# Optimization experiments

Hardware: AMD Instinct MI355X
Metric: run time of the kernel (lower is better)

## Reference

```python
import jax, jax.numpy as jnp
import numpy as np

N_NODES = 50000
N_EDGES = 1_600_000
D_IN, D_HID, D_OUT, K = 128, 50, 10, 5


def setup_inputs() -> dict:
    key = jax.random.key(0)
    ks = jax.random.split(key, 6)
    x = jax.random.normal(ks[0], (N_NODES, D_IN), dtype=jnp.float32)
    edge_index = jax.random.randint(ks[1], (2, N_EDGES), 0, N_NODES, dtype=jnp.int64)
    cheb_w = jax.random.normal(ks[2], (K, D_IN, D_HID), dtype=jnp.float32) * 0.05
    cheb_b = jax.random.normal(ks[3], (D_HID,), dtype=jnp.float32) * 0.05
    fc_w = jax.random.normal(ks[4], (D_HID, D_OUT), dtype=jnp.float32) * 0.1
    fc_b = jax.random.normal(ks[5], (D_OUT,), dtype=jnp.float32) * 0.1
    return {"x": x, "edge_index": edge_index, "cheb_w": cheb_w,
            "cheb_b": cheb_b, "fc_w": fc_w, "fc_b": fc_b}


def reference(x, edge_index, cheb_w, cheb_b, fc_w, fc_b):
    # ChebConv (PyG, normalization='sym', lambda_max=2.0):
    # L_hat = 2L/lambda_max - I = -D^{-1/2} A D^{-1/2} (zero diagonal)
    row, col = edge_index[0], edge_index[1]
    n = x.shape[0]
    deg = jax.ops.segment_sum(jnp.ones_like(row, dtype=x.dtype), row, num_segments=n)
    dinv = jnp.where(deg > 0, jax.lax.rsqrt(jnp.maximum(deg, 1.0)), 0.0)
    w = -dinv[row] * dinv[col]  # [E] edge weights of L_hat

    def prop(h):  # L_hat @ h via gather-scale-scatter
        return jax.ops.segment_sum(w[:, None] * h[col], row, num_segments=n)

    tx0 = x
    tx1 = prop(x)
    out = jnp.einsum('ni,io->no', tx0, cheb_w[0]) + jnp.einsum('ni,io->no', tx1, cheb_w[1])
    for k in range(2, K):
        tx2 = 2.0 * prop(tx1) - tx0
        out = out + jnp.einsum('ni,io->no', tx2, cheb_w[k])
        tx0, tx1 = tx1, tx2
    out = out + cheb_b

    h = jax.nn.relu(out)
    logits = h @ fc_w + fc_b
    return jax.nn.log_softmax(logits, axis=1)
```

## Files before the change

### kernel.cpp

```cpp
#include <hip/hip_runtime.h>
#include <hip/hip_fp16.h>

#define N_NODES 50000
#define N_EDGES 1600000
#define D_IN    128
#define D_HID   50
#define D_OUT   10
#define K_CHEB  5

#define P1_BLOCKS 256
#define EPB       (N_EDGES / P1_BLOCKS)
#define NBUCK     64
#define NB_USED   49
#define BCAP      256

#define WH_ELEMS  (K_CHEB * 64 * D_IN)
#define WH_BLOCKS ((WH_ELEMS + 255) / 256)

#define VROW      64
#define VSTRIDE   ((size_t)(N_NODES + 1) * VROW)

typedef _Float16 half8_t __attribute__((ext_vector_type(8)));
typedef float    f32x4_t __attribute__((ext_vector_type(4)));


__global__ __launch_bounds__(256) void pass1_kernel(const int* __restrict__ row,
                                                    const int* __restrict__ col,
                                                    unsigned int* __restrict__ store,
                                                    int* __restrict__ bcnt,
                                                    const float* __restrict__ W,
                                                    __half* __restrict__ Wh,
                                                    __half* __restrict__ v,
                                                    __half* __restrict__ b1) {
    int tid = threadIdx.x;
    int blk = blockIdx.x;
    if (blk >= P1_BLOCKS) {
        int wb = blk - P1_BLOCKS;
        if (wb < WH_BLOCKS) {
            int idx = wb * 256 + tid;
            if (idx < WH_ELEMS) {
                int i = idx & 127;
                int n = (idx >> 7) & 63;
                int t = idx >> 13;
                float vv = (n < D_HID) ? W[t * D_IN * D_HID + i * D_HID + n] : 0.f;
                Wh[idx] = __float2half(vv);
            }
        } else {
            if (tid < VROW) {
                v[4 * VSTRIDE + (size_t)N_NODES * VROW + tid] = __float2half(0.f);
                b1[(size_t)N_NODES * VROW + tid] = __float2half(0.f);
            }
        }
        return;
    }
    __shared__ int cnt[NBUCK];
    if (tid < NBUCK) cnt[tid] = 0;
    __syncthreads();
    int base = blk * EPB;
    size_t sb = (size_t)blk * (NBUCK * BCAP);
    for (int i = tid; i < EPB; i += 256) {
        int r = row[base + i];
        int c = col[base + i];
        int b = r >> 10;
        int pos = atomicAdd(&cnt[b], 1);
        if (pos >= BCAP) pos = BCAP - 1;
        store[sb + (b << 8) + pos] = ((unsigned int)(r & 1023) << 16) | (unsigned int)c;
    }
    __syncthreads();
    if (tid < NBUCK) bcnt[blk * NBUCK + tid] = cnt[tid];
}

__global__ __launch_bounds__(1024) void pass2_kernel(const unsigned int* __restrict__ store,
                                                     const int* __restrict__ bcnt,
                                                     int* __restrict__ row_start,
                                                     float* __restrict__ dinv,
                                                     float* __restrict__ dinv2,
                                                     float* __restrict__ sdeg,
                                                     int* __restrict__ ewc) {
    __shared__ int hist[1024];
    __shared__ int off[1024];
    __shared__ int fill[1024];
    __shared__ int sb_part[1024];
    __shared__ int pscan[64];
    __shared__ int s_bbase;
    int tid = threadIdx.x;
    int b = blockIdx.x;

    {
        int bt = tid & 63, seg = tid >> 6;
        int sum = 0;
        for (int s = seg * 16; s < seg * 16 + 16; ++s) sum += bcnt[s * NBUCK + bt];
        sb_part[tid] = sum;
    }
    __syncthreads();
    if (tid < 64) {
        int tot = 0;
        #pragma unroll
        for (int seg = 0; seg < 16; ++seg) tot += sb_part[seg * 64 + tid];
        pscan[tid] = tot;
    }
    __syncthreads();
    for (int o = 1; o < 64; o <<= 1) {
        int vv = (tid < 64 && tid >= o) ? pscan[tid - o] : 0;
        __syncthreads();
        if (tid < 64) pscan[tid] += vv;
        __syncthreads();
    }
    if (tid == 0) {
        s_bbase = (b == 0) ? 0 : pscan[b - 1];
        if (b == 0) row_start[N_NODES] = pscan[63];
    }
    hist[tid] = 0;
    __syncthreads();
    int bbase_b = s_bbase;

    int strip = tid >> 2;
    int sub   = tid & 3;
    int sn = bcnt[strip * NBUCK + b];
    size_t sb = (size_t)strip * (NBUCK * BCAP) + (b << 8);
    for (int i = sub; i < sn; i += 4)
        atomicAdd(&hist[store[sb + i] >> 16], 1);
    __syncthreads();
    int d = hist[tid];
    off[tid] = d;
    __syncthreads();
    for (int o = 1; o < 1024; o <<= 1) {
        int vv = (tid >= o) ? off[tid - o] : 0;
        __syncthreads();
        off[tid] += vv;
        __syncthreads();
    }
    int excl = off[tid] - d + bbase_b;
    __syncthreads();
    hist[tid] = excl;
    fill[tid] = 0;
    int r = (b << 10) + tid;
    if (r < N_NODES) {
        row_start[r] = excl;
        float fd = (float)d;
        dinv[r]  = d ? rsqrtf(fd)  : 0.f;
        dinv2[r] = d ? (1.f / fd)  : 0.f;
        sdeg[r]  = d ? sqrtf(fd)   : 0.f;
    }
    __syncthreads();
    for (int i = sub; i < sn; i += 4) {
        unsigned int vv = store[sb + i];
        int rl = vv >> 16;
        int c = vv & 0xffff;
        int p = atomicAdd(&fill[rl], 1);
        ewc[hist[rl] + p] = c;
    }
}

__global__ __launch_bounds__(256) void vgemm_kernel(const float* __restrict__ x,
                                                    const float* __restrict__ dinv,
                                                    const __half* __restrict__ Wh,
                                                    __half* __restrict__ v) {
    int tid = threadIdx.x;
    int lane = tid & 63;
    int wv = __builtin_amdgcn_readfirstlane(tid >> 6);
    int m = lane & 15;
    int quad = lane >> 4;

    int node = (blockIdx.x * 4 + wv) * 16 + m;
    bool ok = (node < N_NODES);
    int ln = ok ? node : (N_NODES - 1);
    float dv = ok ? dinv[node] : 0.f;

    half8_t bfr[4];
    #pragma unroll
    for (int ks = 0; ks < 4; ++ks) {
        const float4* xr = (const float4*)(x + (size_t)ln * D_IN + ks * 32 + quad * 8);
        float4 fA = xr[0], fB = xr[1];
        half8_t h;
        h[0] = (_Float16)fA.x; h[1] = (_Float16)fA.y;
        h[2] = (_Float16)fA.z; h[3] = (_Float16)fA.w;
        h[4] = (_Float16)fB.x; h[5] = (_Float16)fB.y;
        h[6] = (_Float16)fB.z; h[7] = (_Float16)fB.w;
        bfr[ks] = h;
    }

    f32x4_t acc[4];
    #pragma unroll
    for (int jt = 0; jt < 4; ++jt) acc[jt] = (f32x4_t)0.f;

    half8_t aC[4], aN[4];
    #pragma unroll
    for (int jt = 0; jt < 4; ++jt)
        aC[jt] = *(const half8_t*)(Wh + (jt * 16 + m) * D_IN + quad * 8);

    #pragma unroll
    for (int st = 0; st < 20; ++st) {
        int ks = st & 3;
        if (st < 19) {
            int t2 = (st + 1) >> 2, ks2 = (st + 1) & 3;
            const __half* Wn = Wh + t2 * (64 * D_IN);
            int ko2 = ks2 * 32 + quad * 8;
            #pragma unroll
            for (int jt = 0; jt < 4; ++jt)
                aN[jt] = *(const half8_t*)(Wn + (jt * 16 + m) * D_IN + ko2);
        }
        #pragma unroll
        for (int jt = 0; jt < 4; ++jt)
            acc[jt] = __builtin_amdgcn_mfma_f32_16x16x32_f16(aC[jt], bfr[ks], acc[jt], 0, 0, 0);
        if (ks == 3) {
            int t = st >> 2;
            if (ok) {
                __half* dst = v + t * VSTRIDE + (size_t)node * VROW + quad * 4;
                #pragma unroll
                for (int jt = 0; jt < 4; ++jt) {
                    __half2 h0 = __float22half2_rn(make_float2(acc[jt][0] * dv, acc[jt][1] * dv));
                    __half2 h1 = __float22half2_rn(make_float2(acc[jt][2] * dv, acc[jt][3] * dv));
                    uint2 u;
                    u.x = *(unsigned int*)&h0;
                    u.y = *(unsigned int*)&h1;
                    *(uint2*)(dst + jt * 16) = u;
                }
            }
            #pragma unroll
            for (int jt = 0; jt < 4; ++jt) acc[jt] = (f32x4_t)0.f;
        }
        #pragma unroll
        for (int jt = 0; jt < 4; ++jt) aC[jt] = aN[jt];
    }
}

__global__ __launch_bounds__(512) void prop_kernel(const int* __restrict__ row_start,
                                                   const int* __restrict__ ewc,
                                                   const float* __restrict__ dinv2,
                                                   const __half* __restrict__ src,
                                                   const __half* __restrict__ addv,
                                                   const __half* __restrict__ subv,
                                                   float alphaM, int do_sub,
                                                   __half* __restrict__ dst) {
    int tid = threadIdx.x;
    int lane = tid & 63;
    int wv = __builtin_amdgcn_readfirstlane(tid >> 6);
    int r = blockIdx.x * 8 + wv;
    int e0 = row_start[r], e1 = row_start[r + 1];
    float fac = -alphaM * dinv2[r];
    int l = lane & 7;
    int g = lane >> 3;
    const uint4* src16 = (const uint4*)src;
    float ac[8];
    #pragma unroll
    for (int j = 0; j < 8; ++j) ac[j] = 0.f;
    for (int e = e0; e < e1; e += 32) {
        #pragma unroll
        for (int i = 0; i < 4; ++i) {
            int base = e + 8 * i;
            int c0 = ewc[base + 0];
            int c1 = ewc[base + 1];
            int c2 = ewc[base + 2];
            int c3 = ewc[base + 3];
            int c4 = ewc[base + 4];
            int c5 = ewc[base + 5];
            int c6 = ewc[base + 6];
            int c7 = ewc[base + 7];
            int cA = (g & 1) ? c1 : c0;
            int cB = (g & 1) ? c3 : c2;
            int cC = (g & 1) ? c5 : c4;
            int cD = (g & 1) ? c7 : c6;
            int cE = (g & 2) ? cB : cA;
            int cF = (g & 2) ? cD : cC;
            int cl = (g & 4) ? cF : cE;
            if (base + g >= e1) cl = N_NODES;
            uint4 u = src16[(size_t)cl * 8 + l];
            float2 f0 = __half22float2(*(__half2*)&u.x);
            float2 f1 = __half22float2(*(__half2*)&u.y);
            float2 f2 = __half22float2(*(__half2*)&u.z);
            float2 f3 = __half22float2(*(__half2*)&u.w);
            ac[0] += f0.x; ac[1] += f0.y; ac[2] += f1.x; ac[3] += f1.y;
            ac[4] += f2.x; ac[5] += f2.y; ac[6] += f3.x; ac[7] += f3.y;
        }
    }
    #pragma unroll
    for (int k = 8; k <= 32; k <<= 1) {
        #pragma unroll
        for (int j = 0; j < 8; ++j) ac[j] += __shfl_xor(ac[j], k);
    }
    if (g == 0) {
        size_t o = (size_t)r * 8 + l;
        uint4 av = ((const uint4*)addv)[o];
        float2 av0 = __half22float2(*(__half2*)&av.x);
        float2 av1 = __half22float2(*(__half2*)&av.y);
        float2 av2 = __half22float2(*(__half2*)&av.z);
        float2 av3 = __half22float2(*(__half2*)&av.w);
        float r0 = av0.x + fac * ac[0];
        float r1 = av0.y + fac * ac[1];
        float r2 = av1.x + fac * ac[2];
        float r3 = av1.y + fac * ac[3];
        float r4 = av2.x + fac * ac[4];
        float r5 = av2.y + fac * ac[5];
        float r6 = av3.x + fac * ac[6];
        float r7 = av3.y + fac * ac[7];
        if (do_sub) {
            uint4 sv = ((const uint4*)subv)[o];
            float2 sv0 = __half22float2(*(__half2*)&sv.x);
            float2 sv1 = __half22float2(*(__half2*)&sv.y);
            float2 sv2 = __half22float2(*(__half2*)&sv.z);
            float2 sv3 = __half22float2(*(__half2*)&sv.w);
            r0 -= sv0.x; r1 -= sv0.y; r2 -= sv1.x; r3 -= sv1.y;
            r4 -= sv2.x; r5 -= sv2.y; r6 -= sv3.x; r7 -= sv3.y;
        }
        __half2 h0 = __float22half2_rn(make_float2(r0, r1));
        __half2 h1 = __float22half2_rn(make_float2(r2, r3));
        __half2 h2 = __float22half2_rn(make_float2(r4, r5));
        __half2 h3 = __float22half2_rn(make_float2(r6, r7));
        uint4 u;
        u.x = *(unsigned int*)&h0;
        u.y = *(unsigned int*)&h1;
        u.z = *(unsigned int*)&h2;
        u.w = *(unsigned int*)&h3;
        ((uint4*)dst)[o] = u;
    }
}

__global__ __launch_bounds__(256) void final_kernel(const __half* __restrict__ S,
                                                    const float* __restrict__ sdeg,
                                                    const float* __restrict__ cheb_b,
                                                    const float* __restrict__ fc_w,
                                                    const float* __restrict__ fc_b,
                                                    float* __restrict__ out) {
    int r = blockIdx.x * blockDim.x + threadIdx.x;
    if (r >= N_NODES) return;
    float sc = sdeg[r];
    const __half2* s2 = (const __half2*)(S + (size_t)r * VROW);
    float h[D_HID];
    #pragma unroll
    for (int i = 0; i < D_HID / 2; ++i) {
        float2 f = __half22float2(s2[i]);
        float v0 = sc * f.x + cheb_b[2 * i];
        float v1 = sc * f.y + cheb_b[2 * i + 1];
        h[2 * i]     = v0 > 0.f ? v0 : 0.f;
        h[2 * i + 1] = v1 > 0.f ? v1 : 0.f;
    }
    float lg[D_OUT];
    #pragma unroll
    for (int o = 0; o < D_OUT; ++o) lg[o] = fc_b[o];
    #pragma unroll 2
    for (int i = 0; i < D_HID; ++i) {
        float hv = h[i];
        #pragma unroll
        for (int o = 0; o < D_OUT; ++o) lg[o] += hv * fc_w[i * D_OUT + o];
    }
    float mx = lg[0];
    #pragma unroll
    for (int o = 1; o < D_OUT; ++o) mx = fmaxf(mx, lg[o]);
    float s = 0.f;
    #pragma unroll
    for (int o = 0; o < D_OUT; ++o) s += __expf(lg[o] - mx);
    float ls = __logf(s);
    size_t oo = (size_t)r * D_OUT;
    #pragma unroll
    for (int o = 0; o < D_OUT; ++o) out[oo + o] = lg[o] - mx - ls;
}

extern "C" void kernel_launch(void* const* d_in, const int* in_sizes, int n_in,
                              void* d_out, int out_size, void* d_ws, size_t ws_size,
                              hipStream_t stream) {
    const float* x      = (const float*)d_in[0];
    const int*   edge   = (const int*)d_in[1];
    const float* cheb_w = (const float*)d_in[2];
    const float* cheb_b = (const float*)d_in[3];
    const float* fc_w   = (const float*)d_in[4];
    const float* fc_b   = (const float*)d_in[5];
    float* out = (float*)d_out;

    const int* erow = edge;
    const int* ecol = edge + N_EDGES;

    uintptr_t p = ((uintptr_t)d_ws + 255) & ~(uintptr_t)255;
    auto alloc = [&](size_t bytes) {
        uintptr_t q = p;
        p = (p + bytes + 255) & ~(uintptr_t)255;
        return (void*)q;
    };
    unsigned int* store = (unsigned int*)alloc((size_t)P1_BLOCKS * NBUCK * BCAP * 4);
    int*    bcnt      = (int*)alloc((size_t)P1_BLOCKS * NBUCK * 4);
    int*    row_start = (int*)alloc((size_t)(N_NODES + 1) * 4);
    float*  dinv      = (float*)alloc((size_t)N_NODES * 4);
    float*  dinv2     = (float*)alloc((size_t)N_NODES * 4);
    float*  sdeg      = (float*)alloc((size_t)N_NODES * 4);
    int*    ewc       = (int*)alloc((size_t)(N_EDGES + 32) * 4);
    __half* Wh        = (__half*)alloc((size_t)WH_ELEMS * 2);
    __half* Sbuf      = (__half*)alloc(VSTRIDE * 2);
    __half* v         = (__half*)alloc(5 * VSTRIDE * 2);
    __half* b1        = (__half*)alloc(VSTRIDE * 2);

    __half* b3 = (__half*)store;
    __half* b2 = (__half*)store + VSTRIDE;
    __half* S  = Sbuf;

    pass1_kernel<<<P1_BLOCKS + WH_BLOCKS + 1, 256, 0, stream>>>(
        erow, ecol, store, bcnt, cheb_w, Wh, v, b1);
    pass2_kernel<<<NB_USED, 1024, 0, stream>>>(store, bcnt, row_start,
                                               dinv, dinv2, sdeg, ewc);
    hipMemsetAsync(b3 + (size_t)N_NODES * VROW, 0, VROW * 2, stream);
    hipMemsetAsync(b2 + (size_t)N_NODES * VROW, 0, VROW * 2, stream);

    const int GBK = (N_NODES + 63) / 64;
    vgemm_kernel<<<GBK, 256, 0, stream>>>(x, dinv, Wh, v);

    __half* v0 = v;
    __half* v1 = v + 1 * VSTRIDE;
    __half* v2 = v + 2 * VSTRIDE;
    __half* v3 = v + 3 * VSTRIDE;
    __half* v4 = v + 4 * VSTRIDE;
    const int PB = N_NODES / 8;
    prop_kernel<<<PB, 512, 0, stream>>>(row_start, ewc, dinv2, v4, v3, v3, 2.f, 0, b3);
    prop_kernel<<<PB, 512, 0, stream>>>(row_start, ewc, dinv2, b3, v2, v4, 2.f, 1, b2);
    prop_kernel<<<PB, 512, 0, stream>>>(row_start, ewc, dinv2, b2, v1, b3, 2.f, 1, b1);
    prop_kernel<<<PB, 512, 0, stream>>>(row_start, ewc, dinv2, b1, v0, b2, 1.f, 1, S);

    final_kernel<<<(N_NODES + 255) / 256, 256, 0, stream>>>(S, sdeg, cheb_b,
                                                            fc_w, fc_b, out);
}
```

Baseline: 309.1 us.

## Use finer row buckets for CSR build and split vgemm waves per Chebyshev term

The CSR build now uses 256-row buckets (196 blocks of 512 threads) instead of 1024-row buckets (49 blocks of 1024 threads), which puts more blocks to work on the histogram, scan and scatter of the sort pass. The vgemm kernel gives each wave one (16-node group, Chebyshev term) pair instead of looping over all five terms, so it launches five times as many waves, each preloading its full weight slice. This raises parallelism in both stages. In exchange, x rows are reloaded and converted once per term, and bucket capacity drops to 96 entries, which leaves less slack for overflow when a bucket receives more edges than expected.

```diff
diff --git a/kernel.cpp b/kernel.cpp
--- a/kernel.cpp
+++ b/kernel.cpp
@@ -10,9 +10,9 @@
 
 #define P1_BLOCKS 256
 #define EPB       (N_EDGES / P1_BLOCKS)
-#define NBUCK     64
-#define NB_USED   49
-#define BCAP      256
+#define NBUCK2    256
+#define NB_USED2  196
+#define BCAP2     96
 
 #define WH_ELEMS  (K_CHEB * 64 * D_IN)
 #define WH_BLOCKS ((WH_ELEMS + 255) / 256)
@@ -53,97 +53,93 @@
         }
         return;
     }
-    __shared__ int cnt[NBUCK];
-    if (tid < NBUCK) cnt[tid] = 0;
+    __shared__ int cnt[NBUCK2];
+    cnt[tid] = 0;
     __syncthreads();
     int base = blk * EPB;
-    size_t sb = (size_t)blk * (NBUCK * BCAP);
+    size_t sb = (size_t)blk * (NBUCK2 * BCAP2);
     for (int i = tid; i < EPB; i += 256) {
         int r = row[base + i];
         int c = col[base + i];
-        int b = r >> 10;
+        int b = r >> 8;
         int pos = atomicAdd(&cnt[b], 1);
-        if (pos >= BCAP) pos = BCAP - 1;
-        store[sb + (b << 8) + pos] = ((unsigned int)(r & 1023) << 16) | (unsigned int)c;
-    }
-    __syncthreads();
-    if (tid < NBUCK) bcnt[blk * NBUCK + tid] = cnt[tid];
-}
-
-__global__ __launch_bounds__(1024) void pass2_kernel(const unsigned int* __restrict__ store,
-                                                     const int* __restrict__ bcnt,
-                                                     int* __restrict__ row_start,
-                                                     float* __restrict__ dinv,
-                                                     float* __restrict__ dinv2,
-                                                     float* __restrict__ sdeg,
-                                                     int* __restrict__ ewc) {
-    __shared__ int hist[1024];
-    __shared__ int off[1024];
-    __shared__ int fill[1024];
-    __shared__ int sb_part[1024];
-    __shared__ int pscan[64];
+        if (pos >= BCAP2) pos = BCAP2 - 1;
+        store[sb + b * BCAP2 + pos] = ((unsigned int)(r & 255) << 16) | (unsigned int)c;
+    }
+    __syncthreads();
+    bcnt[blk * NBUCK2 + tid] = cnt[tid];
+}
+
+__global__ __launch_bounds__(512) void pass2_kernel(const unsigned int* __restrict__ store,
+                                                    const int* __restrict__ bcnt,
+                                                    int* __restrict__ row_start,
+                                                    float* __restrict__ dinv,
+                                                    float* __restrict__ dinv2,
+                                                    float* __restrict__ sdeg,
+                                                    int* __restrict__ ewc) {
+    __shared__ int hist[256];
+    __shared__ int off[256];
+    __shared__ int fill[256];
+    __shared__ int sb_part[512];
+    __shared__ int pscan[256];
     __shared__ int s_bbase;
     int tid = threadIdx.x;
     int b = blockIdx.x;
 
     {
-        int bt = tid & 63, seg = tid >> 6;
+        int bt = tid & 255, seg = tid >> 8;
         int sum = 0;
-        for (int s = seg * 16; s < seg * 16 + 16; ++s) sum += bcnt[s * NBUCK + bt];
+        for (int s = seg * 128; s < seg * 128 + 128; ++s) sum += bcnt[s * NBUCK2 + bt];
         sb_part[tid] = sum;
     }
     __syncthreads();
-    if (tid < 64) {
-        int tot = 0;
-        #pragma unroll
-        for (int seg = 0; seg < 16; ++seg) tot += sb_part[seg * 64 + tid];
-        pscan[tid] = tot;
-    }
-    __syncthreads();
-    for (int o = 1; o < 64; o <<= 1) {
-        int vv = (tid < 64 && tid >= o) ? pscan[tid - o] : 0;
+    if (tid < 256) pscan[tid] = sb_part[tid] + sb_part[256 + tid];
+    __syncthreads();
+    for (int o = 1; o < 256; o <<= 1) {
+        int vv = (tid < 256 && tid >= o) ? pscan[tid - o] : 0;
         __syncthreads();
-        if (tid < 64) pscan[tid] += vv;
+        if (tid < 256) pscan[tid] += vv;
         __syncthreads();
     }
     if (tid == 0) {
         s_bbase = (b == 0) ? 0 : pscan[b - 1];
-        if (b == 0) row_start[N_NODES] = pscan[63];
-    }
-    hist[tid] = 0;
+        if (b == 0) row_start[N_NODES] = pscan[255];
+    }
+    if (tid < 256) hist[tid] = 0;
     __syncthreads();
     int bbase_b = s_bbase;
 
-    int strip = tid >> 2;
-    int sub   = tid & 3;
-    int sn = bcnt[strip * NBUCK + b];
-    size_t sb = (size_t)strip * (NBUCK * BCAP) + (b << 8);
-    for (int i = sub; i < sn; i += 4)
+    int strip = tid >> 1;
+    int sub   = tid & 1;
+    int sn = bcnt[strip * NBUCK2 + b];
+    size_t sb = (size_t)strip * (NBUCK2 * BCAP2) + b * BCAP2;
+    for (int i = sub; i < sn; i += 2)
         atomicAdd(&hist[store[sb + i] >> 16], 1);
     __syncthreads();
-    int d = hist[tid];
-    off[tid] = d;
-    __syncthreads();
-    for (int o = 1; o < 1024; o <<= 1) {
-        int vv = (tid >= o) ? off[tid - o] : 0;
+    int d = (tid < 256) ? hist[tid] : 0;
+    if (tid < 256) off[tid] = d;
+    __syncthreads();
+    for (int o = 1; o < 256; o <<= 1) {
+        int vv = (tid < 256 && tid >= o) ? off[tid - o] : 0;
         __syncthreads();
-        off[tid] += vv;
+        if (tid < 256) off[tid] += vv;
         __syncthreads();
     }
-    int excl = off[tid] - d + bbase_b;
-    __syncthreads();
-    hist[tid] = excl;
-    fill[tid] = 0;
-    int r = (b << 10) + tid;
-    if (r < N_NODES) {
-        row_start[r] = excl;
-        float fd = (float)d;
-        dinv[r]  = d ? rsqrtf(fd)  : 0.f;
-        dinv2[r] = d ? (1.f / fd)  : 0.f;
-        sdeg[r]  = d ? sqrtf(fd)   : 0.f;
-    }
-    __syncthreads();
-    for (int i = sub; i < sn; i += 4) {
+    if (tid < 256) {
+        int excl = off[tid] - d + bbase_b;
+        hist[tid] = excl;
+        fill[tid] = 0;
+        int r = (b << 8) + tid;
+        if (r < N_NODES) {
+            row_start[r] = excl;
+            float fd = (float)d;
+            dinv[r]  = d ? rsqrtf(fd)  : 0.f;
+            dinv2[r] = d ? (1.f / fd)  : 0.f;
+            sdeg[r]  = d ? sqrtf(fd)   : 0.f;
+        }
+    }
+    __syncthreads();
+    for (int i = sub; i < sn; i += 2) {
         unsigned int vv = store[sb + i];
         int rl = vv >> 16;
         int c = vv & 0xffff;
@@ -159,10 +155,13 @@
     int tid = threadIdx.x;
     int lane = tid & 63;
     int wv = __builtin_amdgcn_readfirstlane(tid >> 6);
+    int w = blockIdx.x * 4 + wv;
+    int grp = w / 5;
+    int t = w - grp * 5;
     int m = lane & 15;
     int quad = lane >> 4;
 
-    int node = (blockIdx.x * 4 + wv) * 16 + m;
+    int node = grp * 16 + m;
     bool ok = (node < N_NODES);
     int ln = ok ? node : (N_NODES - 1);
     float dv = ok ? dinv[node] : 0.f;
@@ -180,48 +179,36 @@
         bfr[ks] = h;
     }
 
+    const __half* Wt = Wh + t * (64 * D_IN);
+    half8_t afr[4][4];
+    #pragma unroll
+    for (int ks = 0; ks < 4; ++ks) {
+        int ko = ks * 32 + quad * 8;
+        #pragma unroll
+        for (int jt = 0; jt < 4; ++jt)
+            afr[ks][jt] = *(const half8_t*)(Wt + (jt * 16 + m) * D_IN + ko);
+    }
+
     f32x4_t acc[4];
     #pragma unroll
     for (int jt = 0; jt < 4; ++jt) acc[jt] = (f32x4_t)0.f;
-
-    half8_t aC[4], aN[4];
-    #pragma unroll
-    for (int jt = 0; jt < 4; ++jt)
-        aC[jt] = *(const half8_t*)(Wh + (jt * 16 + m) * D_IN + quad * 8);
-
-    #pragma unroll
-    for (int st = 0; st < 20; ++st) {
-        int ks = st & 3;
-        if (st < 19) {
-            int t2 = (st + 1) >> 2, ks2 = (st + 1) & 3;
-            const __half* Wn = Wh + t2 * (64 * D_IN);
-            int ko2 = ks2 * 32 + quad * 8;
-            #pragma unroll
-            for (int jt = 0; jt < 4; ++jt)
-                aN[jt] = *(const half8_t*)(Wn + (jt * 16 + m) * D_IN + ko2);
+    #pragma unroll
+    for (int ks = 0; ks < 4; ++ks)
+        #pragma unroll
+        for (int jt = 0; jt < 4; ++jt)
+            acc[jt] = __builtin_amdgcn_mfma_f32_16x16x32_f16(afr[ks][jt], bfr[ks], acc[jt], 0, 0, 0);
+
+    if (ok) {
+        __half* dst = v + t * VSTRIDE + (size_t)node * VROW + quad * 4;
+        #pragma unroll
+        for (int jt = 0; jt < 4; ++jt) {
+            __half2 h0 = __float22half2_rn(make_float2(acc[jt][0] * dv, acc[jt][1] * dv));
+            __half2 h1 = __float22half2_rn(make_float2(acc[jt][2] * dv, acc[jt][3] * dv));
+            uint2 u;
+            u.x = *(unsigned int*)&h0;
+            u.y = *(unsigned int*)&h1;
+            *(uint2*)(dst + jt * 16) = u;
         }
-        #pragma unroll
-        for (int jt = 0; jt < 4; ++jt)
-            acc[jt] = __builtin_amdgcn_mfma_f32_16x16x32_f16(aC[jt], bfr[ks], acc[jt], 0, 0, 0);
-        if (ks == 3) {
-            int t = st >> 2;
-            if (ok) {
-                __half* dst = v + t * VSTRIDE + (size_t)node * VROW + quad * 4;
-                #pragma unroll
-                for (int jt = 0; jt < 4; ++jt) {
-                    __half2 h0 = __float22half2_rn(make_float2(acc[jt][0] * dv, acc[jt][1] * dv));
-                    __half2 h1 = __float22half2_rn(make_float2(acc[jt][2] * dv, acc[jt][3] * dv));
-                    uint2 u;
-                    u.x = *(unsigned int*)&h0;
-                    u.y = *(unsigned int*)&h1;
-                    *(uint2*)(dst + jt * 16) = u;
-                }
-            }
-            #pragma unroll
-            for (int jt = 0; jt < 4; ++jt) acc[jt] = (f32x4_t)0.f;
-        }
-        #pragma unroll
-        for (int jt = 0; jt < 4; ++jt) aC[jt] = aN[jt];
     }
 }
 
@@ -376,8 +363,8 @@
         p = (p + bytes + 255) & ~(uintptr_t)255;
         return (void*)q;
     };
-    unsigned int* store = (unsigned int*)alloc((size_t)P1_BLOCKS * NBUCK * BCAP * 4);
-    int*    bcnt      = (int*)alloc((size_t)P1_BLOCKS * NBUCK * 4);
+    unsigned int* store = (unsigned int*)alloc((size_t)P1_BLOCKS * NBUCK2 * BCAP2 * 4);
+    int*    bcnt      = (int*)alloc((size_t)P1_BLOCKS * NBUCK2 * 4);
     int*    row_start = (int*)alloc((size_t)(N_NODES + 1) * 4);
     float*  dinv      = (float*)alloc((size_t)N_NODES * 4);
     float*  dinv2     = (float*)alloc((size_t)N_NODES * 4);
@@ -394,12 +381,13 @@
 
     pass1_kernel<<<P1_BLOCKS + WH_BLOCKS + 1, 256, 0, stream>>>(
         erow, ecol, store, bcnt, cheb_w, Wh, v, b1);
-    pass2_kernel<<<NB_USED, 1024, 0, stream>>>(store, bcnt, row_start,
+    pass2_kernel<<<NB_USED2, 512, 0, stream>>>(store, bcnt, row_start,
                                                dinv, dinv2, sdeg, ewc);
     hipMemsetAsync(b3 + (size_t)N_NODES * VROW, 0, VROW * 2, stream);
     hipMemsetAsync(b2 + (size_t)N_NODES * VROW, 0, VROW * 2, stream);
 
-    const int GBK = (N_NODES + 63) / 64;
+    const int NWAVE = ((N_NODES + 15) / 16) * K_CHEB;
+    const int GBK = (NWAVE + 3) / 4;
     vgemm_kernel<<<GBK, 256, 0, stream>>>(x, dinv, Wh, v);
 
     __half* v0 = v;
```

After: 311.6 us. No clear change (+0.8%).
